# Kernel optimization log

Hardware: AMD Instinct MI355X
Metric: run time of the kernel (lower is better)

## Reference

```python
import jax, jax.numpy as jnp
import numpy as np

EMB = 1024
HEADS = 16
HEAD_SZ = EMB // HEADS
EPS = 1e-5


def _layernorm(x, g, b):
    mu = jnp.mean(x, axis=-1, keepdims=True)
    var = jnp.mean(jnp.square(x - mu), axis=-1, keepdims=True)
    return (x - mu) * jax.lax.rsqrt(var + EPS) * g + b


def setup_inputs() -> dict:
    key = jax.random.key(0)
    ks = jax.random.split(key, 12)
    s_in = 1.0 / np.sqrt(EMB)
    s_h = 1.0 / np.sqrt(4 * EMB)
    return {
        "x": jax.random.normal(ks[0], (4, 1024, EMB), jnp.float32),
        # per-head Q/K/V projections stacked: [H, EMB, HEAD_SZ], no bias
        "wq": jax.random.normal(ks[1], (HEADS, EMB, HEAD_SZ), jnp.float32) * s_in,
        "wk": jax.random.normal(ks[2], (HEADS, EMB, HEAD_SZ), jnp.float32) * s_in,
        "wv": jax.random.normal(ks[3], (HEADS, EMB, HEAD_SZ), jnp.float32) * s_in,
        "w_proj": jax.random.normal(ks[4], (EMB, EMB), jnp.float32) * s_in,
        "b_proj": jnp.zeros((EMB,), jnp.float32),
        "w1": jax.random.normal(ks[5], (EMB, 4 * EMB), jnp.float32) * s_in,
        "b1": jnp.zeros((4 * EMB,), jnp.float32),
        "w2": jax.random.normal(ks[6], (4 * EMB, EMB), jnp.float32) * s_h,
        "b2": jnp.zeros((EMB,), jnp.float32),
        "g1": jnp.ones((EMB,), jnp.float32),
        "be1": jnp.zeros((EMB,), jnp.float32),
        "g2": jnp.ones((EMB,), jnp.float32),
        "be2": jnp.zeros((EMB,), jnp.float32),
    }


def reference(x, wq, wk, wv, w_proj, b_proj, w1, b1, w2, b2, g1, be1, g2, be2):
    B, T, C = x.shape
    # --- self-attention (pre-norm) ---
    h = _layernorm(x, g1, be1)
    q = jnp.einsum("btc,hcd->bhtd", h, wq)
    k = jnp.einsum("btc,hcd->bhtd", h, wk)
    v = jnp.einsum("btc,hcd->bhtd", h, wv)
    scale = 1.0 / jnp.sqrt(jnp.asarray(HEAD_SZ, x.dtype))
    scores = jnp.einsum("bhtd,bhsd->bhts", q, k) * scale  # non-causal: SDPA called with no mask
    attn = jax.nn.softmax(scores, axis=-1)
    o = jnp.einsum("bhts,bhsd->bhtd", attn, v)
    o = o.transpose(0, 2, 1, 3).reshape(B, T, C)  # concat heads (same order as torch.cat)
    sa_out = o @ w_proj + b_proj
    x = x + sa_out
    # --- feed-forward; note ln2 applied twice, faithful to source ---
    t = _layernorm(x, g2, be2)
    t = _layernorm(t, g2, be2)
    ff = jax.nn.relu(t @ w1 + b1) @ w2 + b2
    return x + ff
```

## Files before the change

### kernel.cpp

```cpp
#include <hip/hip_runtime.h>
#include <hip/hip_bf16.h>
#include <math.h>
#include <stdint.h>

typedef __bf16 bf16_t;
typedef __bf16 bf16x4 __attribute__((ext_vector_type(4)));
typedef __bf16 bf16x8 __attribute__((ext_vector_type(8)));
typedef float floatx4 __attribute__((ext_vector_type(4)));

#define BM 128
#define BK 32

__device__ __forceinline__ size_t ftaddr(int m, int k, int KT) {
    return ((size_t)(m >> 4) * KT + (k >> 5)) * 512
         + (((k >> 3) & 3) * 16 + (m & 15)) * 8 + (k & 7);
}

__device__ __forceinline__ void gload16(const void* g, void* lds) {
    __builtin_amdgcn_global_load_lds(
        (__attribute__((address_space(1))) void*)(uintptr_t)g,
        (__attribute__((address_space(3))) void*)(uintptr_t)lds,
        16, 0, 0);
}

__global__ void transpose_all(const float* __restrict__ wq, const float* __restrict__ wk,
                              const float* __restrict__ wv, const float* __restrict__ w_proj,
                              const float* __restrict__ w1, const float* __restrict__ w2,
                              bf16_t* __restrict__ WQKVT, bf16_t* __restrict__ WPROJT,
                              bf16_t* __restrict__ W1T, bf16_t* __restrict__ W2T)
{
    const int idx = blockIdx.x;
    const float* in; bf16_t* out; int R, C, rt, ct; long nrow0;
    if (idx < 768) {
        const int z = idx >> 8;
        const int hd = (idx >> 4) & 15;
        rt = idx & 15; ct = 0; R = 1024; C = 64;
        in  = (z == 0 ? wq : z == 1 ? wk : wv) + hd * 65536;
        out = WQKVT; nrow0 = z * 1024 + hd * 64;
    } else if (idx < 1024) {
        const int t = idx - 768; rt = t & 15; ct = t >> 4; R = 1024; C = 1024;
        in = w_proj; out = WPROJT; nrow0 = 0;
    } else if (idx < 2048) {
        const int t = idx - 1024; rt = t & 15; ct = t >> 4; R = 1024; C = 4096;
        in = w1; out = W1T; nrow0 = 0;
    } else {
        const int t = idx - 2048; rt = t & 63; ct = t >> 6; R = 4096; C = 1024;
        in = w2; out = W2T; nrow0 = 0;
    }
    __shared__ float tile[64][65];
    const int tid = threadIdx.x;
    const int r0 = rt * 64, c0 = ct * 64;
    const int tr = tid >> 4;
    const int tc = (tid & 15) * 4;
#pragma unroll
    for (int rr = 0; rr < 4; rr++) {
        const int r = tr + rr * 16;
        const float4 v = *(const float4*)&in[(long)(r0 + r) * C + c0 + tc];
        tile[r][tc + 0] = v.x; tile[r][tc + 1] = v.y;
        tile[r][tc + 2] = v.z; tile[r][tc + 3] = v.w;
    }
    __syncthreads();
    const int KT = R >> 5;
#pragma unroll
    for (int rr = 0; rr < 4; rr++) {
        const int c = tr + rr * 16;
        const long n = nrow0 + c0 + c;
        const int k = r0 + tc;
        bf16x4 o;
        o[0] = (bf16_t)tile[tc + 0][c];
        o[1] = (bf16_t)tile[tc + 1][c];
        o[2] = (bf16_t)tile[tc + 2][c];
        o[3] = (bf16_t)tile[tc + 3][c];
        *(bf16x4*)&out[ftaddr((int)n, k, KT)] = o;
    }
}

__global__ void ln_kernel(const float* __restrict__ x, const float* __restrict__ g,
                          const float* __restrict__ b, bf16_t* __restrict__ outb)
{
    const int row = blockIdx.x;
    const int tid = threadIdx.x;
    const float4 v = ((const float4*)(x + (long)row * 1024))[tid];
    float s  = v.x + v.y + v.z + v.w;
    float s2 = v.x * v.x + v.y * v.y + v.z * v.z + v.w * v.w;
#pragma unroll
    for (int off = 32; off >= 1; off >>= 1) {
        s  += __shfl_xor(s, off);
        s2 += __shfl_xor(s2, off);
    }
    __shared__ float red[8];
    const int wv = tid >> 6;
    if ((tid & 63) == 0) { red[wv] = s; red[4 + wv] = s2; }
    __syncthreads();
    s  = red[0] + red[1] + red[2] + red[3];
    s2 = red[4] + red[5] + red[6] + red[7];
    const float mu  = s * (1.0f / 1024.0f);
    const float var = fmaxf(s2 * (1.0f / 1024.0f) - mu * mu, 0.0f);
    const float rs  = rsqrtf(var + 1e-5f);
    const float4 gv = ((const float4*)g)[tid];
    const float4 bv = ((const float4*)b)[tid];
    bf16x4 o;
    o[0] = (bf16_t)((v.x - mu) * rs * gv.x + bv.x);
    o[1] = (bf16_t)((v.y - mu) * rs * gv.y + bv.y);
    o[2] = (bf16_t)((v.z - mu) * rs * gv.z + bv.z);
    o[3] = (bf16_t)((v.w - mu) * rs * gv.w + bv.w);
    *(bf16x4*)&outb[ftaddr(row, tid * 4, 32)] = o;
}

__global__ void ln2x_kernel(const float* __restrict__ x, const float* __restrict__ g,
                            const float* __restrict__ b, bf16_t* __restrict__ outb)
{
    const int row = blockIdx.x;
    const int tid = threadIdx.x;
    const float4 v = ((const float4*)(x + (long)row * 1024))[tid];
    float s  = v.x + v.y + v.z + v.w;
    float s2 = v.x * v.x + v.y * v.y + v.z * v.z + v.w * v.w;
#pragma unroll
    for (int off = 32; off >= 1; off >>= 1) {
        s  += __shfl_xor(s, off);
        s2 += __shfl_xor(s2, off);
    }
    __shared__ float red[8];
    __shared__ float red2[8];
    const int wv = tid >> 6;
    if ((tid & 63) == 0) { red[wv] = s; red[4 + wv] = s2; }
    __syncthreads();
    s  = red[0] + red[1] + red[2] + red[3];
    s2 = red[4] + red[5] + red[6] + red[7];
    float mu  = s * (1.0f / 1024.0f);
    float var = fmaxf(s2 * (1.0f / 1024.0f) - mu * mu, 0.0f);
    float rs  = rsqrtf(var + 1e-5f);
    const float4 gv = ((const float4*)g)[tid];
    const float4 bv = ((const float4*)b)[tid];
    float y0 = (v.x - mu) * rs * gv.x + bv.x;
    float y1 = (v.y - mu) * rs * gv.y + bv.y;
    float y2 = (v.z - mu) * rs * gv.z + bv.z;
    float y3 = (v.w - mu) * rs * gv.w + bv.w;
    s  = y0 + y1 + y2 + y3;
    s2 = y0 * y0 + y1 * y1 + y2 * y2 + y3 * y3;
#pragma unroll
    for (int off = 32; off >= 1; off >>= 1) {
        s  += __shfl_xor(s, off);
        s2 += __shfl_xor(s2, off);
    }
    if ((tid & 63) == 0) { red2[wv] = s; red2[4 + wv] = s2; }
    __syncthreads();
    s  = red2[0] + red2[1] + red2[2] + red2[3];
    s2 = red2[4] + red2[5] + red2[6] + red2[7];
    mu  = s * (1.0f / 1024.0f);
    var = fmaxf(s2 * (1.0f / 1024.0f) - mu * mu, 0.0f);
    rs  = rsqrtf(var + 1e-5f);
    bf16x4 o;
    o[0] = (bf16_t)((y0 - mu) * rs * gv.x + bv.x);
    o[1] = (bf16_t)((y1 - mu) * rs * gv.y + bv.y);
    o[2] = (bf16_t)((y2 - mu) * rs * gv.z + bv.z);
    o[3] = (bf16_t)((y3 - mu) * rs * gv.w + bv.w);
    *(bf16x4*)&outb[ftaddr(row, tid * 4, 32)] = o;
}

template<int EPI, int BNt>
__global__ __launch_bounds__(256, 2)
void gemm_bt(const bf16_t* __restrict__ A, const bf16_t* __restrict__ Bt,
             const int K,
             const float* __restrict__ bias, const float* __restrict__ resid,
             float* __restrict__ outf, bf16_t* __restrict__ outb,
             bf16_t* __restrict__ aux1, bf16_t* __restrict__ aux2,
             const int Nout)
{
    constexpr int NFRAG = BNt / 16;
    __shared__ __align__(16) bf16_t As[3][8 * 512];
    __shared__ __align__(16) bf16_t Bs[3][NFRAG * 512];
    const int tid  = threadIdx.x;
    const int wave = tid >> 6, lane = tid & 63;
    const int bm = blockIdx.x * BM, bn = blockIdx.y * BNt;
    const int KT = K >> 5;

    floatx4 acc[2][NFRAG];
#pragma unroll
    for (int i = 0; i < 2; i++)
#pragma unroll
        for (int j = 0; j < NFRAG; j++) acc[i][j] = (floatx4){0.f, 0.f, 0.f, 0.f};

    const bf16_t* gA0 = A + ((size_t)(bm / 16 + wave * 2 + 0) * KT) * 512 + lane * 8;
    const bf16_t* gA1 = A + ((size_t)(bm / 16 + wave * 2 + 1) * KT) * 512 + lane * 8;
    const int lA0 = (wave * 2 + 0) * 512;
    const int lA1 = (wave * 2 + 1) * 512;

    const bf16_t* gB0;
    const bf16_t* gB1 = nullptr;
    int lB0, lB1 = 0;
    if (BNt == 128) {
        gB0 = Bt + ((size_t)(bn / 16 + wave * 2 + 0) * KT) * 512 + lane * 8;
        gB1 = Bt + ((size_t)(bn / 16 + wave * 2 + 1) * KT) * 512 + lane * 8;
        lB0 = (wave * 2 + 0) * 512;
        lB1 = (wave * 2 + 1) * 512;
    } else {
        gB0 = Bt + ((size_t)(bn / 16 + wave) * KT) * 512 + lane * 8;
        lB0 = wave * 512;
    }

    auto stage = [&](int t, int bu) {
        const size_t off = (size_t)t * 512;
        gload16(gA0 + off, (bf16_t*)As[bu] + lA0);
        gload16(gA1 + off, (bf16_t*)As[bu] + lA1);
        gload16(gB0 + off, (bf16_t*)Bs[bu] + lB0);
        if (BNt == 128) gload16(gB1 + off, (bf16_t*)Bs[bu] + lB1);
    };

    auto compute = [&](int bu) {
        bf16x8 af[2], bfv[NFRAG];
#pragma unroll
        for (int i = 0; i < 2; i++)
            af[i] = *(const bf16x8*)&As[bu][(wave * 2 + i) * 512 + lane * 8];
#pragma unroll
        for (int j = 0; j < NFRAG; j++)
            bfv[j] = *(const bf16x8*)&Bs[bu][j * 512 + lane * 8];
#pragma unroll
        for (int i = 0; i < 2; i++)
#pragma unroll
            for (int j = 0; j < NFRAG; j++)
                acc[i][j] = __builtin_amdgcn_mfma_f32_16x16x32_bf16(af[i], bfv[j], acc[i][j], 0, 0, 0);
    };

    const int NT = K / BK;
    stage(0, 0);
    stage(1, 1);
    int bu = 0;
    for (int t = 0; t < NT - 1; ++t) {
        if (BNt == 128) asm volatile("s_waitcnt vmcnt(4)\n\ts_barrier" ::: "memory");
        else            asm volatile("s_waitcnt vmcnt(3)\n\ts_barrier" ::: "memory");
        if (t + 2 < NT) stage(t + 2, (t + 2) % 3);
        compute(bu);
        bu = (bu + 1) % 3;
    }
    asm volatile("s_waitcnt vmcnt(0)\n\ts_barrier" ::: "memory");
    compute(bu);

    const int er = (lane >> 4) * 4, ec = lane & 15;
#pragma unroll
    for (int i = 0; i < 2; i++) {
#pragma unroll
        for (int j = 0; j < NFRAG; j++) {
            const int col = bn + j * 16 + ec;
#pragma unroll
            for (int r = 0; r < 4; r++) {
                const int row = bm + wave * 32 + i * 16 + er + r;
                const float v = acc[i][j][r];
                if (EPI == 0) {
                    const int b = row >> 10, t = row & 1023;
                    if (col < 1024) {
                        const int h = col >> 6, d = col & 63;
                        outb[(size_t)((b * 16 + h) * 1024 + t) * 64 + d] = (bf16_t)v;
                    } else if (col < 2048) {
                        const int c2 = col - 1024, h = c2 >> 6, d = c2 & 63;
                        aux1[(size_t)((b * 16 + h) * 1024 + t) * 64 + d] = (bf16_t)v;
                    } else {
                        const int c2 = col - 2048, h = c2 >> 6, d = c2 & 63;
                        aux2[(size_t)((b * 16 + h) * 64 + d) * 1024 + t] = (bf16_t)v;
                    }
                } else if (EPI == 1 || EPI == 3) {
                    const size_t idx = (size_t)row * Nout + col;
                    outf[idx] = v + bias[col] + resid[idx];
                } else if (EPI == 2) {
                    outb[ftaddr(row, col, Nout >> 5)] = (bf16_t)fmaxf(v + bias[col], 0.f);
                }
            }
        }
    }
}

__global__ __launch_bounds__(256, 4)
void attn_kernel(const bf16_t* __restrict__ Q, const bf16_t* __restrict__ Kg,
                 const bf16_t* __restrict__ Vt, bf16_t* __restrict__ Og)
{
    __shared__ __align__(16) bf16_t Ks[2][4096];
    __shared__ __align__(16) bf16_t Vs[2][4096];
    __shared__ __align__(16) bf16_t Ps[4][1024];
    const int tid = threadIdx.x, wave = tid >> 6, lane = tid & 63;
    const int bh = blockIdx.y;
    const int b = bh >> 4, h = bh & 15;
    const int q0 = blockIdx.x * 64 + wave * 16;
    const bf16_t* Qb = Q + (size_t)bh * 65536;
    const char* Kb = (const char*)(Kg + (size_t)bh * 65536);
    const char* Vb = (const char*)(Vt + (size_t)bh * 65536);
    const int fr = lane & 15, g = lane >> 4, fk = g * 8;

    const bf16x8 qf0 = *(const bf16x8*)&Qb[(size_t)(q0 + fr) * 64 + fk];
    const bf16x8 qf1 = *(const bf16x8*)&Qb[(size_t)(q0 + fr) * 64 + 32 + fk];

    floatx4 o[4];
#pragma unroll
    for (int dt = 0; dt < 4; dt++) o[dt] = (floatx4){0.f, 0.f, 0.f, 0.f};
    float lsum[4] = {0.f, 0.f, 0.f, 0.f};
    bf16_t* pw = &Ps[wave][0];
    const float sscale = 0.125f * 1.44269504088896f;

    auto stage = [&](int s0, int bu) {
#pragma unroll
        for (int t = 0; t < 2; t++) {
            const int j = wave * 2 + t;
            gload16(Kb + (size_t)(s0 + lane) * 128 + j * 16, &Ks[bu][j * 512]);
            gload16(Vb + (size_t)lane * 2048 + (size_t)s0 * 2 + j * 16, &Vs[bu][j * 512]);
        }
    };

    stage(0, 0);
    int bu = 0;
    for (int it = 0; it < 16; ++it) {
        __syncthreads();
        if (it < 15) stage((it + 1) * 64, bu ^ 1);
        const bf16_t* Kl = Ks[bu];
        const bf16_t* Vl = Vs[bu];

        floatx4 sacc[4];
#pragma unroll
        for (int ss = 0; ss < 4; ss++) sacc[ss] = (floatx4){0.f, 0.f, 0.f, 0.f};
#pragma unroll
        for (int c = 0; c < 2; c++) {
            const int ch = c * 4 + g;
            const bf16x8 qf = (c == 0) ? qf0 : qf1;
#pragma unroll
            for (int ss = 0; ss < 4; ss++) {
                const bf16x8 kf = *(const bf16x8*)&Kl[ch * 512 + (ss * 16 + fr) * 8];
                sacc[ss] = __builtin_amdgcn_mfma_f32_16x16x32_bf16(qf, kf, sacc[ss], 0, 0, 0);
            }
        }
#pragma unroll
        for (int ss = 0; ss < 4; ss++) {
#pragma unroll
            for (int r = 0; r < 4; r++) {
                const float p = __builtin_amdgcn_exp2f(sacc[ss][r] * sscale);
                lsum[r] += p;
                const int q = g * 4 + r;
                pw[(ss * 2 + (fr >> 3)) * 128 + q * 8 + (fr & 7)] = (bf16_t)p;
            }
        }
        asm volatile("s_waitcnt lgkmcnt(0)" ::: "memory");
#pragma unroll
        for (int c = 0; c < 2; c++) {
            const int ch = c * 4 + g;
            const bf16x8 pf = *(const bf16x8*)&pw[ch * 128 + fr * 8];
#pragma unroll
            for (int dt = 0; dt < 4; dt++) {
                const bf16x8 vf = *(const bf16x8*)&Vl[ch * 512 + (dt * 16 + fr) * 8];
                o[dt] = __builtin_amdgcn_mfma_f32_16x16x32_bf16(pf, vf, o[dt], 0, 0, 0);
            }
        }
        asm volatile("" ::: "memory");
        bu ^= 1;
    }
#pragma unroll
    for (int r = 0; r < 4; r++) {
        float l = lsum[r];
        l += __shfl_xor(l, 1);
        l += __shfl_xor(l, 2);
        l += __shfl_xor(l, 4);
        l += __shfl_xor(l, 8);
        lsum[r] = 1.0f / l;
    }
    const int tq = q0 + g * 4;
#pragma unroll
    for (int dt = 0; dt < 4; dt++) {
#pragma unroll
        for (int r = 0; r < 4; r++) {
            const int m = b * 1024 + tq + r;
            const int k = h * 64 + dt * 16 + fr;
            Og[ftaddr(m, k, 32)] = (bf16_t)(o[dt][r] * lsum[r]);
        }
    }
}

extern "C" void kernel_launch(void* const* d_in, const int* in_sizes, int n_in,
                              void* d_out, int out_size, void* d_ws, size_t ws_size,
                              hipStream_t stream)
{
    const float* x      = (const float*)d_in[0];
    const float* wq     = (const float*)d_in[1];
    const float* wk     = (const float*)d_in[2];
    const float* wv     = (const float*)d_in[3];
    const float* w_proj = (const float*)d_in[4];
    const float* b_proj = (const float*)d_in[5];
    const float* w1     = (const float*)d_in[6];
    const float* b1     = (const float*)d_in[7];
    const float* w2     = (const float*)d_in[8];
    const float* b2     = (const float*)d_in[9];
    const float* g1     = (const float*)d_in[10];
    const float* be1    = (const float*)d_in[11];
    const float* g2     = (const float*)d_in[12];
    const float* be2    = (const float*)d_in[13];
    float* out = (float*)d_out;
    char* ws = (char*)d_ws;

    bf16_t* WQKVT = (bf16_t*)(ws + 0x0000000);
    bf16_t* WPROJT= (bf16_t*)(ws + 0x0600000);
    bf16_t* W1T   = (bf16_t*)(ws + 0x0800000);
    bf16_t* W2T   = (bf16_t*)(ws + 0x1000000);
    bf16_t* HB    = (bf16_t*)(ws + 0x1800000);
    bf16_t* Qb    = (bf16_t*)(ws + 0x2000000);
    bf16_t* Kb    = (bf16_t*)(ws + 0x2800000);
    bf16_t* Vtb   = (bf16_t*)(ws + 0x3000000);
    bf16_t* AO    = (bf16_t*)(ws + 0x3800000);
    float*  X2    = (float*)(ws + 0x4000000);
    bf16_t* TB    = (bf16_t*)(ws + 0x2800000);
    bf16_t* FF1B  = (bf16_t*)(ws + 0x5000000);

    dim3 blk(256);
    transpose_all<<<3072, blk, 0, stream>>>(wq, wk, wv, w_proj, w1, w2,
                                            WQKVT, WPROJT, W1T, W2T);
    ln_kernel<<<4096, blk, 0, stream>>>(x, g1, be1, HB);
    gemm_bt<0, 128><<<dim3(32, 24), blk, 0, stream>>>(HB, WQKVT, 1024, nullptr, nullptr,
                                                      nullptr, Qb, Kb, Vtb, 3072);
    attn_kernel<<<dim3(16, 64), blk, 0, stream>>>(Qb, Kb, Vtb, AO);
    gemm_bt<1, 64><<<dim3(32, 16), blk, 0, stream>>>(AO, WPROJT, 1024, b_proj, x,
                                                     X2, nullptr, nullptr, nullptr, 1024);
    ln2x_kernel<<<4096, blk, 0, stream>>>(X2, g2, be2, TB);
    gemm_bt<2, 128><<<dim3(32, 32), blk, 0, stream>>>(TB, W1T, 1024, b1, nullptr,
                                                      nullptr, FF1B, nullptr, nullptr, 4096);
    gemm_bt<3, 64><<<dim3(32, 16), blk, 0, stream>>>(FF1B, W2T, 4096, b2, X2,
                                                     out, nullptr, nullptr, nullptr, 1024);
}
```

Before: 318.9 us.

## Stage layernorm output in LDS for coalesced tiled stores; widen transpose writes

```diff
diff --git a/kernel.cpp b/kernel.cpp
--- a/kernel.cpp
+++ b/kernel.cpp
@@ -61,101 +61,138 @@
     }
     __syncthreads();
     const int KT = R >> 5;
-#pragma unroll
-    for (int rr = 0; rr < 4; rr++) {
-        const int c = tr + rr * 16;
-        const long n = nrow0 + c0 + c;
-        const int k = r0 + tc;
-        bf16x4 o;
-        o[0] = (bf16_t)tile[tc + 0][c];
-        o[1] = (bf16_t)tile[tc + 1][c];
-        o[2] = (bf16_t)tile[tc + 2][c];
-        o[3] = (bf16_t)tile[tc + 3][c];
-        *(bf16x4*)&out[ftaddr((int)n, k, KT)] = o;
+    const int w = tid >> 6, l = tid & 63;
+    const int c = l >> 4, rr = l & 15;
+#pragma unroll
+    for (int it = 0; it < 2; ++it) {
+        const int t8 = it * 4 + w;
+        const int kt = t8 >> 2;
+        const int nb = t8 & 3;
+        const long n = nrow0 + c0 + nb * 16 + rr;
+        const int k = r0 + kt * 32 + c * 8;
+        bf16x8 o;
+#pragma unroll
+        for (int e = 0; e < 8; e++)
+            o[e] = (bf16_t)tile[kt * 32 + c * 8 + e][nb * 16 + rr];
+        *(bf16x8*)&out[ftaddr((int)n, k, KT)] = o;
     }
 }
 
 __global__ void ln_kernel(const float* __restrict__ x, const float* __restrict__ g,
                           const float* __restrict__ b, bf16_t* __restrict__ outb)
 {
-    const int row = blockIdx.x;
-    const int tid = threadIdx.x;
-    const float4 v = ((const float4*)(x + (long)row * 1024))[tid];
-    float s  = v.x + v.y + v.z + v.w;
-    float s2 = v.x * v.x + v.y * v.y + v.z * v.z + v.w * v.w;
-#pragma unroll
-    for (int off = 32; off >= 1; off >>= 1) {
-        s  += __shfl_xor(s, off);
-        s2 += __shfl_xor(s2, off);
-    }
-    __shared__ float red[8];
-    const int wv = tid >> 6;
-    if ((tid & 63) == 0) { red[wv] = s; red[4 + wv] = s2; }
+    __shared__ __align__(16) bf16_t ybuf[16][1032];
+    const int tid = threadIdx.x, wave = tid >> 6, lane = tid & 63;
+    const int rb = blockIdx.x;
+    float4 gvv[4], bvv[4];
+#pragma unroll
+    for (int j = 0; j < 4; j++) {
+        gvv[j] = ((const float4*)g)[lane + j * 64];
+        bvv[j] = ((const float4*)b)[lane + j * 64];
+    }
+    for (int rr = 0; rr < 4; ++rr) {
+        const int lrow = wave * 4 + rr;
+        const float* xr = x + (size_t)(rb * 16 + lrow) * 1024;
+        float4 v[4];
+        float s = 0.f, s2 = 0.f;
+#pragma unroll
+        for (int j = 0; j < 4; j++) {
+            v[j] = ((const float4*)xr)[lane + j * 64];
+            s  += v[j].x + v[j].y + v[j].z + v[j].w;
+            s2 += v[j].x * v[j].x + v[j].y * v[j].y + v[j].z * v[j].z + v[j].w * v[j].w;
+        }
+#pragma unroll
+        for (int off = 32; off >= 1; off >>= 1) {
+            s  += __shfl_xor(s, off);
+            s2 += __shfl_xor(s2, off);
+        }
+        const float mu = s * (1.0f / 1024.0f);
+        const float rs = rsqrtf(fmaxf(s2 * (1.0f / 1024.0f) - mu * mu, 0.f) + 1e-5f);
+#pragma unroll
+        for (int j = 0; j < 4; j++) {
+            bf16x4 o;
+            o[0] = (bf16_t)((v[j].x - mu) * rs * gvv[j].x + bvv[j].x);
+            o[1] = (bf16_t)((v[j].y - mu) * rs * gvv[j].y + bvv[j].y);
+            o[2] = (bf16_t)((v[j].z - mu) * rs * gvv[j].z + bvv[j].z);
+            o[3] = (bf16_t)((v[j].w - mu) * rs * gvv[j].w + bvv[j].w);
+            *(bf16x4*)&ybuf[lrow][(lane + j * 64) * 4] = o;
+        }
+    }
     __syncthreads();
-    s  = red[0] + red[1] + red[2] + red[3];
-    s2 = red[4] + red[5] + red[6] + red[7];
-    const float mu  = s * (1.0f / 1024.0f);
-    const float var = fmaxf(s2 * (1.0f / 1024.0f) - mu * mu, 0.0f);
-    const float rs  = rsqrtf(var + 1e-5f);
-    const float4 gv = ((const float4*)g)[tid];
-    const float4 bv = ((const float4*)b)[tid];
-    bf16x4 o;
-    o[0] = (bf16_t)((v.x - mu) * rs * gv.x + bv.x);
-    o[1] = (bf16_t)((v.y - mu) * rs * gv.y + bv.y);
-    o[2] = (bf16_t)((v.z - mu) * rs * gv.z + bv.z);
-    o[3] = (bf16_t)((v.w - mu) * rs * gv.w + bv.w);
-    *(bf16x4*)&outb[ftaddr(row, tid * 4, 32)] = o;
+    bf16_t* outBase = outb + (size_t)rb * 32 * 512;
+    for (int it = 0; it < 8; ++it) {
+        const int s = it * 256 + tid;
+        const int kt = s >> 6, c = (s >> 4) & 3, rr = s & 15;
+        const bf16x8 val = *(const bf16x8*)&ybuf[rr][kt * 32 + c * 8];
+        *(bf16x8*)&outBase[(size_t)s * 8] = val;
+    }
 }
 
 __global__ void ln2x_kernel(const float* __restrict__ x, const float* __restrict__ g,
                             const float* __restrict__ b, bf16_t* __restrict__ outb)
 {
-    const int row = blockIdx.x;
-    const int tid = threadIdx.x;
-    const float4 v = ((const float4*)(x + (long)row * 1024))[tid];
-    float s  = v.x + v.y + v.z + v.w;
-    float s2 = v.x * v.x + v.y * v.y + v.z * v.z + v.w * v.w;
-#pragma unroll
-    for (int off = 32; off >= 1; off >>= 1) {
-        s  += __shfl_xor(s, off);
-        s2 += __shfl_xor(s2, off);
-    }
-    __shared__ float red[8];
-    __shared__ float red2[8];
-    const int wv = tid >> 6;
-    if ((tid & 63) == 0) { red[wv] = s; red[4 + wv] = s2; }
+    __shared__ __align__(16) bf16_t ybuf[16][1032];
+    const int tid = threadIdx.x, wave = tid >> 6, lane = tid & 63;
+    const int rb = blockIdx.x;
+    float4 gvv[4], bvv[4];
+#pragma unroll
+    for (int j = 0; j < 4; j++) {
+        gvv[j] = ((const float4*)g)[lane + j * 64];
+        bvv[j] = ((const float4*)b)[lane + j * 64];
+    }
+    for (int rr = 0; rr < 4; ++rr) {
+        const int lrow = wave * 4 + rr;
+        const float* xr = x + (size_t)(rb * 16 + lrow) * 1024;
+        float4 v[4];
+        float s = 0.f, s2 = 0.f;
+#pragma unroll
+        for (int j = 0; j < 4; j++) {
+            v[j] = ((const float4*)xr)[lane + j * 64];
+            s  += v[j].x + v[j].y + v[j].z + v[j].w;
+            s2 += v[j].x * v[j].x + v[j].y * v[j].y + v[j].z * v[j].z + v[j].w * v[j].w;
+        }
+#pragma unroll
+        for (int off = 32; off >= 1; off >>= 1) {
+            s  += __shfl_xor(s, off);
+            s2 += __shfl_xor(s2, off);
+        }
+        float mu = s * (1.0f / 1024.0f);
+        float rs = rsqrtf(fmaxf(s2 * (1.0f / 1024.0f) - mu * mu, 0.f) + 1e-5f);
+        s = 0.f; s2 = 0.f;
+#pragma unroll
+        for (int j = 0; j < 4; j++) {
+            v[j].x = (v[j].x - mu) * rs * gvv[j].x + bvv[j].x;
+            v[j].y = (v[j].y - mu) * rs * gvv[j].y + bvv[j].y;
+            v[j].z = (v[j].z - mu) * rs * gvv[j].z + bvv[j].z;
+            v[j].w = (v[j].w - mu) * rs * gvv[j].w + bvv[j].w;
+            s  += v[j].x + v[j].y + v[j].z + v[j].w;
+            s2 += v[j].x * v[j].x + v[j].y * v[j].y + v[j].z * v[j].z + v[j].w * v[j].w;
+        }
+#pragma unroll
+        for (int off = 32; off >= 1; off >>= 1) {
+            s  += __shfl_xor(s, off);
+            s2 += __shfl_xor(s2, off);
+        }
+        mu = s * (1.0f / 1024.0f);
+        rs = rsqrtf(fmaxf(s2 * (1.0f / 1024.0f) - mu * mu, 0.f) + 1e-5f);
+#pragma unroll
+        for (int j = 0; j < 4; j++) {
+            bf16x4 o;
+            o[0] = (bf16_t)((v[j].x - mu) * rs * gvv[j].x + bvv[j].x);
+            o[1] = (bf16_t)((v[j].y - mu) * rs * gvv[j].y + bvv[j].y);
+            o[2] = (bf16_t)((v[j].z - mu) * rs * gvv[j].z + bvv[j].z);
+            o[3] = (bf16_t)((v[j].w - mu) * rs * gvv[j].w + bvv[j].w);
+            *(bf16x4*)&ybuf[lrow][(lane + j * 64) * 4] = o;
+        }
+    }
     __syncthreads();
-    s  = red[0] + red[1] + red[2] + red[3];
-    s2 = red[4] + red[5] + red[6] + red[7];
-    float mu  = s * (1.0f / 1024.0f);
-    float var = fmaxf(s2 * (1.0f / 1024.0f) - mu * mu, 0.0f);
-    float rs  = rsqrtf(var + 1e-5f);
-    const float4 gv = ((const float4*)g)[tid];
-    const float4 bv = ((const float4*)b)[tid];
-    float y0 = (v.x - mu) * rs * gv.x + bv.x;
-    float y1 = (v.y - mu) * rs * gv.y + bv.y;
-    float y2 = (v.z - mu) * rs * gv.z + bv.z;
-    float y3 = (v.w - mu) * rs * gv.w + bv.w;
-    s  = y0 + y1 + y2 + y3;
-    s2 = y0 * y0 + y1 * y1 + y2 * y2 + y3 * y3;
-#pragma unroll
-    for (int off = 32; off >= 1; off >>= 1) {
-        s  += __shfl_xor(s, off);
-        s2 += __shfl_xor(s2, off);
-    }
-    if ((tid & 63) == 0) { red2[wv] = s; red2[4 + wv] = s2; }
-    __syncthreads();
-    s  = red2[0] + red2[1] + red2[2] + red2[3];
-    s2 = red2[4] + red2[5] + red2[6] + red2[7];
-    mu  = s * (1.0f / 1024.0f);
-    var = fmaxf(s2 * (1.0f / 1024.0f) - mu * mu, 0.0f);
-    rs  = rsqrtf(var + 1e-5f);
-    bf16x4 o;
-    o[0] = (bf16_t)((y0 - mu) * rs * gv.x + bv.x);
-    o[1] = (bf16_t)((y1 - mu) * rs * gv.y + bv.y);
-    o[2] = (bf16_t)((y2 - mu) * rs * gv.z + bv.z);
-    o[3] = (bf16_t)((y3 - mu) * rs * gv.w + bv.w);
-    *(bf16x4*)&outb[ftaddr(row, tid * 4, 32)] = o;
+    bf16_t* outBase = outb + (size_t)rb * 32 * 512;
+    for (int it = 0; it < 8; ++it) {
+        const int s = it * 256 + tid;
+        const int kt = s >> 6, c = (s >> 4) & 3, rr = s & 15;
+        const bf16x8 val = *(const bf16x8*)&ybuf[rr][kt * 32 + c * 8];
+        *(bf16x8*)&outBase[(size_t)s * 8] = val;
+    }
 }
 
 template<int EPI, int BNt>
@@ -407,13 +444,13 @@
     dim3 blk(256);
     transpose_all<<<3072, blk, 0, stream>>>(wq, wk, wv, w_proj, w1, w2,
                                             WQKVT, WPROJT, W1T, W2T);
-    ln_kernel<<<4096, blk, 0, stream>>>(x, g1, be1, HB);
+    ln_kernel<<<256, blk, 0, stream>>>(x, g1, be1, HB);
     gemm_bt<0, 128><<<dim3(32, 24), blk, 0, stream>>>(HB, WQKVT, 1024, nullptr, nullptr,
                                                       nullptr, Qb, Kb, Vtb, 3072);
     attn_kernel<<<dim3(16, 64), blk, 0, stream>>>(Qb, Kb, Vtb, AO);
     gemm_bt<1, 64><<<dim3(32, 16), blk, 0, stream>>>(AO, WPROJT, 1024, b_proj, x,
                                                      X2, nullptr, nullptr, nullptr, 1024);
-    ln2x_kernel<<<4096, blk, 0, stream>>>(X2, g2, be2, TB);
+    ln2x_kernel<<<256, blk, 0, stream>>>(X2, g2, be2, TB);
     gemm_bt<2, 128><<<dim3(32, 32), blk, 0, stream>>>(TB, W1T, 1024, b1, nullptr,
                                                       nullptr, FF1B, nullptr, nullptr, 4096);
     gemm_bt<3, 64><<<dim3(32, 16), blk, 0, stream>>>(FF1B, W2T, 4096, b2, X2,
```

Result: no change. 316.8 us (-0.7%).
